# Performance work log

Measured on AMD Instinct MI355X. Metric: run time of the kernel, lower is better.

## Reference

```python
import jax, jax.numpy as jnp
import numpy as np

EPS_RMS = 1e-6
EPS_Q = 1e-5


def _weight_quant(w):
    # BitNet b1.58-style ternary weight quantization with mean-abs scale
    scale = 1.0 / jnp.clip(jnp.mean(jnp.abs(w)), EPS_Q)
    wq = jnp.clip(jnp.round(w * scale), -1.0, 1.0) / scale
    return w + jax.lax.stop_gradient(wq - w)  # STE


def _activation_quant(x):
    # per-token 8-bit absmax quantization
    scale = 127.0 / jnp.clip(jnp.max(jnp.abs(x), axis=-1, keepdims=True), EPS_Q)
    xq = jnp.clip(jnp.round(x * scale), -128.0, 127.0) / scale
    return x + jax.lax.stop_gradient(xq - x)  # STE


def _rmsnorm(x, weight):
    inv = jax.lax.rsqrt(jnp.mean(x * x, axis=-1, keepdims=True) + EPS_RMS)
    return x * inv * weight


def setup_inputs() -> dict:
    key = jax.random.key(0)
    k1, k2, k3 = jax.random.split(key, 3)
    B, S, D, CD = 8, 4096, 1024, 1024
    x = jax.random.normal(k1, (B, S, D), dtype=jnp.float32)
    c = jax.random.normal(k2, (B, CD), dtype=jnp.float32)
    # NOTE: the module zero-inits proj; we use small random weights so the
    # quantized conditioning path is numerically exercised.
    w_proj = jax.random.normal(k3, (2 * D, CD), dtype=jnp.float32) * 0.02
    b_proj = jnp.zeros((2 * D,), dtype=jnp.float32)
    rms_weight = jnp.ones((D,), dtype=jnp.float32)
    return {"x": x, "c": c, "w_proj": w_proj, "b_proj": b_proj, "rms_weight": rms_weight}


def reference(x, c, w_proj, b_proj, rms_weight):
    if c.ndim == 2:
        c = c[:, None, :]  # [B, 1, cond_dim]
    # BitLinear: quantized activations x quantized ternary weights
    cq = _activation_quant(c)
    wq = _weight_quant(w_proj)
    emb = jnp.einsum('btc,dc->btd', cq, wq) + b_proj  # [B, 1, 2*dim]
    scale, shift = jnp.split(emb, 2, axis=-1)
    xn = _rmsnorm(x, rms_weight)
    return xn * (1.0 + scale) + shift
```

## Files before the change

### kernel.cpp

```cpp
#include <hip/hip_runtime.h>
#include <math.h>


constexpr int Bn = 8;
constexpr int Dn = 1024;
constexpr int TWO_D = 2048;
constexpr int OFF_PART = 0;
constexpr int OFF_CQ   = 4096;
constexpr int OFF_G    = 16384;
constexpr int OFF_SH   = 24576;

using f4 = __attribute__((ext_vector_type(4))) float;

__device__ __forceinline__ float wsumf(float v) {
#pragma unroll
    for (int o = 32; o > 0; o >>= 1) v += __shfl_xor(v, o, 64);
    return v;
}
__device__ __forceinline__ float wmaxf(float v) {
#pragma unroll
    for (int o = 32; o > 0; o >>= 1) v = fmaxf(v, __shfl_xor(v, o, 64));
    return v;
}
__device__ __forceinline__ float qclip(float v, float s, float lo, float hi) {
    return fminf(fmaxf(rintf(v * s), lo), hi);
}
__device__ __forceinline__ float maxabs4(f4 v) {
    return fmaxf(fmaxf(fabsf(v.x), fabsf(v.y)), fmaxf(fabsf(v.z), fabsf(v.w)));
}
__device__ __forceinline__ float sumsq4(f4 v) {
    return v.x*v.x + v.y*v.y + v.z*v.z + v.w*v.w;
}

__global__ void k_pre(const float* __restrict__ w, const float* __restrict__ c,
                      float* __restrict__ part, float* __restrict__ cq) {
    int tid = threadIdx.x;
    if (blockIdx.x < TWO_D) {
        f4 v = *(const f4*)(w + (size_t)blockIdx.x * 1024 + (size_t)tid * 4);
        float s = wsumf(fabsf(v.x) + fabsf(v.y) + fabsf(v.z) + fabsf(v.w));
        __shared__ float lds[4];
        if ((tid & 63) == 0) lds[tid >> 6] = s;
        __syncthreads();
        if (tid == 0) part[blockIdx.x] = lds[0] + lds[1] + lds[2] + lds[3];
    } else {
        int b = blockIdx.x - TWO_D;
        f4 v = ((const f4*)(c + (size_t)b * Dn))[tid];
        float m = wmaxf(maxabs4(v));
        __shared__ float lm[4];
        if ((tid & 63) == 0) lm[tid >> 6] = m;
        __syncthreads();
        float mx = fmaxf(fmaxf(lm[0], lm[1]), fmaxf(lm[2], lm[3]));
        float scale = 127.0f / fmaxf(mx, 1e-5f);
        float inv = 1.0f / scale;
        f4 q;
        q.x = qclip(v.x, scale, -128.f, 127.f) * inv;
        q.y = qclip(v.y, scale, -128.f, 127.f) * inv;
        q.z = qclip(v.z, scale, -128.f, 127.f) * inv;
        q.w = qclip(v.w, scale, -128.f, 127.f) * inv;
        ((f4*)(cq + (size_t)b * Dn))[tid] = q;
    }
}

__global__ void k_emb(const float* __restrict__ w, const float* __restrict__ bp,
                      const float* __restrict__ cq, const float* __restrict__ part,
                      const float* __restrict__ rw,
                      float* __restrict__ g, float* __restrict__ sh) {
    int tid = threadIdx.x;
    float s = 0.0f;
#pragma unroll
    for (int k = 0; k < 8; ++k) s += part[tid + k * 256];
    s = wsumf(s);
    __shared__ float lds[4];
    if ((tid & 63) == 0) lds[tid >> 6] = s;
    __syncthreads();
    float mw = fmaxf((lds[0] + lds[1] + lds[2] + lds[3]) * (1.0f / 2097152.0f), 1e-5f);
    float sw = 1.0f / mw;

    int lane = tid & 63;
    int d = (blockIdx.x * blockDim.x + tid) >> 6;
    const float* wr = w + (size_t)d * 1024 + (size_t)lane * 16;
    float t[16];
#pragma unroll
    for (int j = 0; j < 16; j += 4) {
        f4 v = *(const f4*)(wr + j);
        t[j + 0] = qclip(v.x, sw, -1.f, 1.f);
        t[j + 1] = qclip(v.y, sw, -1.f, 1.f);
        t[j + 2] = qclip(v.z, sw, -1.f, 1.f);
        t[j + 3] = qclip(v.w, sw, -1.f, 1.f);
    }
    float acc[Bn];
#pragma unroll
    for (int b = 0; b < Bn; ++b) {
        const float* cr = cq + (size_t)b * Dn + (size_t)lane * 16;
        float dot = 0.0f;
#pragma unroll
        for (int j = 0; j < 16; j += 4) {
            f4 u = *(const f4*)(cr + j);
            dot += t[j + 0] * u.x + t[j + 1] * u.y + t[j + 2] * u.z + t[j + 3] * u.w;
        }
        acc[b] = dot;
    }
#pragma unroll
    for (int o = 32; o > 0; o >>= 1) {
#pragma unroll
        for (int b = 0; b < Bn; ++b) acc[b] += __shfl_xor(acc[b], o, 64);
    }
    if (lane == 0) {
        float bias = bp[d];
        if (d < Dn) {
            float rwd = rw[d];
#pragma unroll
            for (int b = 0; b < Bn; ++b)
                g[b * Dn + d] = rwd * (1.0f + (acc[b] * mw + bias));
        } else {
#pragma unroll
            for (int b = 0; b < Bn; ++b)
                sh[b * Dn + (d - Dn)] = acc[b] * mw + bias;
        }
    }
}

__global__ void __launch_bounds__(256) k_main(
        const float* __restrict__ x, const float* __restrict__ g,
        const float* __restrict__ sh, float* __restrict__ out) {
    int tid  = threadIdx.x;
    int lane = tid & 63;
    int row0 = (blockIdx.x * 4 + (tid >> 6)) * 4;
    int b    = row0 >> 12;

    const f4* gv = (const f4*)(g  + (size_t)b * Dn);
    const f4* hv = (const f4*)(sh + (size_t)b * Dn);
    f4 g0 = gv[lane], g1 = gv[lane+64], g2 = gv[lane+128], g3 = gv[lane+192];
    f4 h0 = hv[lane], h1 = hv[lane+64], h2 = hv[lane+128], h3 = hv[lane+192];

#pragma unroll
    for (int p = 0; p < 2; ++p) {
        int row = row0 + p * 2;
        const f4* xa = (const f4*)(x + (size_t)row * Dn);
        const f4* xb = xa + 256;
        f4 a0 = xa[lane], a1 = xa[lane+64], a2 = xa[lane+128], a3 = xa[lane+192];
        f4 b0 = xb[lane], b1 = xb[lane+64], b2 = xb[lane+128], b3 = xb[lane+192];
        float sa = sumsq4(a0) + sumsq4(a1) + sumsq4(a2) + sumsq4(a3);
        float sb = sumsq4(b0) + sumsq4(b1) + sumsq4(b2) + sumsq4(b3);
#pragma unroll
        for (int o = 32; o > 0; o >>= 1) {
            sa += __shfl_xor(sa, o, 64);
            sb += __shfl_xor(sb, o, 64);
        }
        float ia = rsqrtf(sa * (1.0f / 1024.0f) + 1e-6f);
        float ib = rsqrtf(sb * (1.0f / 1024.0f) + 1e-6f);
        f4* oa = (f4*)(out + (size_t)row * Dn);
        f4* ob = oa + 256;
        f4 o0;
        o0.x = a0.x*ia*g0.x + h0.x; o0.y = a0.y*ia*g0.y + h0.y;
        o0.z = a0.z*ia*g0.z + h0.z; o0.w = a0.w*ia*g0.w + h0.w;
        oa[lane] = o0;
        o0.x = a1.x*ia*g1.x + h1.x; o0.y = a1.y*ia*g1.y + h1.y;
        o0.z = a1.z*ia*g1.z + h1.z; o0.w = a1.w*ia*g1.w + h1.w;
        oa[lane+64] = o0;
        o0.x = a2.x*ia*g2.x + h2.x; o0.y = a2.y*ia*g2.y + h2.y;
        o0.z = a2.z*ia*g2.z + h2.z; o0.w = a2.w*ia*g2.w + h2.w;
        oa[lane+128] = o0;
        o0.x = a3.x*ia*g3.x + h3.x; o0.y = a3.y*ia*g3.y + h3.y;
        o0.z = a3.z*ia*g3.z + h3.z; o0.w = a3.w*ia*g3.w + h3.w;
        oa[lane+192] = o0;
        o0.x = b0.x*ib*g0.x + h0.x; o0.y = b0.y*ib*g0.y + h0.y;
        o0.z = b0.z*ib*g0.z + h0.z; o0.w = b0.w*ib*g0.w + h0.w;
        ob[lane] = o0;
        o0.x = b1.x*ib*g1.x + h1.x; o0.y = b1.y*ib*g1.y + h1.y;
        o0.z = b1.z*ib*g1.z + h1.z; o0.w = b1.w*ib*g1.w + h1.w;
        ob[lane+64] = o0;
        o0.x = b2.x*ib*g2.x + h2.x; o0.y = b2.y*ib*g2.y + h2.y;
        o0.z = b2.z*ib*g2.z + h2.z; o0.w = b2.w*ib*g2.w + h2.w;
        ob[lane+128] = o0;
        o0.x = b3.x*ib*g3.x + h3.x; o0.y = b3.y*ib*g3.y + h3.y;
        o0.z = b3.z*ib*g3.z + h3.z; o0.w = b3.w*ib*g3.w + h3.w;
        ob[lane+192] = o0;
    }
}

extern "C" void kernel_launch(void* const* d_in, const int* in_sizes, int n_in,
                              void* d_out, int out_size, void* d_ws, size_t ws_size,
                              hipStream_t stream) {
    const float* x  = (const float*)d_in[0];
    const float* c  = (const float*)d_in[1];
    const float* w  = (const float*)d_in[2];
    const float* bp = (const float*)d_in[3];
    const float* rw = (const float*)d_in[4];
    float* out = (float*)d_out;
    float* ws  = (float*)d_ws;

    float* part = ws + OFF_PART;
    float* cq   = ws + OFF_CQ;
    float* g    = ws + OFF_G;
    float* sh   = ws + OFF_SH;

    k_pre <<<TWO_D + Bn, 256, 0, stream>>>(w, c, part, cq);
    k_emb <<<TWO_D / 4, 256, 0, stream>>>(w, bp, cq, part, rw, g, sh);
    k_main<<<2048, 256, 0, stream>>>(x, g, sh, out);
}
```

Measured before the change: 61.04 us.

## Fuse three kernels into one cooperative kernel with grid-wide syncs

Merges the weight-abs partial sum, activation quantization, embedding projection and the main RMSNorm/modulation pass into a single cooperative launch of 2048 blocks separated by two grid.sync barriers. The three-kernel path is kept as a fallback when occupancy is too low or the cooperative launch fails. The aim is to remove two kernel launch gaps. In exchange it adds grid-barrier cost, an occupancy query on every call, and a launch-bounds hint that may constrain registers in the main phase.

After: 62.05 us. No clear change (+1.6%).

```diff
diff --git a/kernel.cpp b/kernel.cpp
--- a/kernel.cpp
+++ b/kernel.cpp
@@ -1,17 +1,22 @@
 #include <hip/hip_runtime.h>
+#include <hip/hip_cooperative_groups.h>
 #include <math.h>
 
+namespace cg = cooperative_groups;
+
+using f4 = __attribute__((ext_vector_type(4))) float;
 
 constexpr int Bn = 8;
 constexpr int Dn = 1024;
 constexpr int TWO_D = 2048;
+constexpr int NTHR = 256;
+constexpr int NBLK = 2048;
+
 constexpr int OFF_PART = 0;
 constexpr int OFF_CQ   = 4096;
 constexpr int OFF_G    = 16384;
 constexpr int OFF_SH   = 24576;
 
-using f4 = __attribute__((ext_vector_type(4))) float;
-
 __device__ __forceinline__ float wsumf(float v) {
 #pragma unroll
     for (int o = 32; o > 0; o >>= 1) v += __shfl_xor(v, o, 64);
@@ -32,61 +37,66 @@
     return v.x*v.x + v.y*v.y + v.z*v.z + v.w*v.w;
 }
 
-__global__ void k_pre(const float* __restrict__ w, const float* __restrict__ c,
-                      float* __restrict__ part, float* __restrict__ cq) {
+
+__device__ __forceinline__ void phase_wpart(const float* __restrict__ w,
+                                            float* __restrict__ part, int ch) {
     int tid = threadIdx.x;
-    if (blockIdx.x < TWO_D) {
-        f4 v = *(const f4*)(w + (size_t)blockIdx.x * 1024 + (size_t)tid * 4);
-        float s = wsumf(fabsf(v.x) + fabsf(v.y) + fabsf(v.z) + fabsf(v.w));
-        __shared__ float lds[4];
-        if ((tid & 63) == 0) lds[tid >> 6] = s;
-        __syncthreads();
-        if (tid == 0) part[blockIdx.x] = lds[0] + lds[1] + lds[2] + lds[3];
-    } else {
-        int b = blockIdx.x - TWO_D;
-        f4 v = ((const f4*)(c + (size_t)b * Dn))[tid];
-        float m = wmaxf(maxabs4(v));
-        __shared__ float lm[4];
-        if ((tid & 63) == 0) lm[tid >> 6] = m;
-        __syncthreads();
-        float mx = fmaxf(fmaxf(lm[0], lm[1]), fmaxf(lm[2], lm[3]));
-        float scale = 127.0f / fmaxf(mx, 1e-5f);
-        float inv = 1.0f / scale;
-        f4 q;
-        q.x = qclip(v.x, scale, -128.f, 127.f) * inv;
-        q.y = qclip(v.y, scale, -128.f, 127.f) * inv;
-        q.z = qclip(v.z, scale, -128.f, 127.f) * inv;
-        q.w = qclip(v.w, scale, -128.f, 127.f) * inv;
-        ((f4*)(cq + (size_t)b * Dn))[tid] = q;
-    }
-}
-
-__global__ void k_emb(const float* __restrict__ w, const float* __restrict__ bp,
-                      const float* __restrict__ cq, const float* __restrict__ part,
-                      const float* __restrict__ rw,
-                      float* __restrict__ g, float* __restrict__ sh) {
+    __shared__ float lds[4];
+    f4 v = *(const f4*)(w + (size_t)ch * 1024 + (size_t)tid * 4);
+    float s = wsumf(fabsf(v.x) + fabsf(v.y) + fabsf(v.z) + fabsf(v.w));
+    if ((tid & 63) == 0) lds[tid >> 6] = s;
+    __syncthreads();
+    if (tid == 0) part[ch] = lds[0] + lds[1] + lds[2] + lds[3];
+    __syncthreads();
+}
+
+__device__ __forceinline__ void phase_cq(const float* __restrict__ c,
+                                         float* __restrict__ cq, int b) {
     int tid = threadIdx.x;
+    __shared__ float lm[4];
+    f4 v = ((const f4*)(c + (size_t)b * Dn))[tid];
+    float m = wmaxf(maxabs4(v));
+    if ((tid & 63) == 0) lm[tid >> 6] = m;
+    __syncthreads();
+    float mx = fmaxf(fmaxf(lm[0], lm[1]), fmaxf(lm[2], lm[3]));
+    float scale = 127.0f / fmaxf(mx, 1e-5f);
+    float inv = 1.0f / scale;
+    f4 q;
+    q.x = qclip(v.x, scale, -128.f, 127.f) * inv;
+    q.y = qclip(v.y, scale, -128.f, 127.f) * inv;
+    q.z = qclip(v.z, scale, -128.f, 127.f) * inv;
+    q.w = qclip(v.w, scale, -128.f, 127.f) * inv;
+    ((f4*)(cq + (size_t)b * Dn))[tid] = q;
+}
+
+__device__ __forceinline__ void phase_emb(const float* __restrict__ w,
+                                          const float* __restrict__ bp,
+                                          const float* __restrict__ cq,
+                                          const float* __restrict__ part,
+                                          const float* __restrict__ rw,
+                                          float* __restrict__ g,
+                                          float* __restrict__ sh, int blk) {
+    int tid = threadIdx.x, lane = tid & 63, widx = tid >> 6;
+    __shared__ float lds2[4];
     float s = 0.0f;
 #pragma unroll
     for (int k = 0; k < 8; ++k) s += part[tid + k * 256];
     s = wsumf(s);
-    __shared__ float lds[4];
-    if ((tid & 63) == 0) lds[tid >> 6] = s;
-    __syncthreads();
-    float mw = fmaxf((lds[0] + lds[1] + lds[2] + lds[3]) * (1.0f / 2097152.0f), 1e-5f);
+    if (lane == 0) lds2[widx] = s;
+    __syncthreads();
+    float mw = fmaxf((lds2[0]+lds2[1]+lds2[2]+lds2[3]) * (1.0f / 2097152.0f), 1e-5f);
     float sw = 1.0f / mw;
 
-    int lane = tid & 63;
-    int d = (blockIdx.x * blockDim.x + tid) >> 6;
-    const float* wr = w + (size_t)d * 1024 + (size_t)lane * 16;
+    int d = blk * 4 + widx;
+    const float* wr = w + (size_t)d * Dn + (size_t)lane * 16;
     float t[16];
 #pragma unroll
     for (int j = 0; j < 16; j += 4) {
         f4 v = *(const f4*)(wr + j);
-        t[j + 0] = qclip(v.x, sw, -1.f, 1.f);
-        t[j + 1] = qclip(v.y, sw, -1.f, 1.f);
-        t[j + 2] = qclip(v.z, sw, -1.f, 1.f);
-        t[j + 3] = qclip(v.w, sw, -1.f, 1.f);
+        t[j+0] = qclip(v.x, sw, -1.f, 1.f);
+        t[j+1] = qclip(v.y, sw, -1.f, 1.f);
+        t[j+2] = qclip(v.z, sw, -1.f, 1.f);
+        t[j+3] = qclip(v.w, sw, -1.f, 1.f);
     }
     float acc[Bn];
 #pragma unroll
@@ -96,7 +106,7 @@
 #pragma unroll
         for (int j = 0; j < 16; j += 4) {
             f4 u = *(const f4*)(cr + j);
-            dot += t[j + 0] * u.x + t[j + 1] * u.y + t[j + 2] * u.z + t[j + 3] * u.w;
+            dot += t[j+0]*u.x + t[j+1]*u.y + t[j+2]*u.z + t[j+3]*u.w;
         }
         acc[b] = dot;
     }
@@ -120,14 +130,12 @@
     }
 }
 
-__global__ void __launch_bounds__(256) k_main(
-        const float* __restrict__ x, const float* __restrict__ g,
-        const float* __restrict__ sh, float* __restrict__ out) {
-    int tid  = threadIdx.x;
-    int lane = tid & 63;
-    int row0 = (blockIdx.x * 4 + (tid >> 6)) * 4;
-    int b    = row0 >> 12;
-
+__device__ __forceinline__ void phase_main(const float* __restrict__ x,
+                                           const float* __restrict__ g,
+                                           const float* __restrict__ sh,
+                                           float* __restrict__ out,
+                                           int row0, int lane) {
+    int b = row0 >> 12;
     const f4* gv = (const f4*)(g  + (size_t)b * Dn);
     const f4* hv = (const f4*)(sh + (size_t)b * Dn);
     f4 g0 = gv[lane], g1 = gv[lane+64], g2 = gv[lane+128], g3 = gv[lane+192];
@@ -179,6 +187,49 @@
     }
 }
 
+
+__global__ void __launch_bounds__(NTHR, 8) k_fused(
+    const float* __restrict__ x, const float* __restrict__ c,
+    const float* __restrict__ w, const float* __restrict__ bp,
+    const float* __restrict__ rw, float* __restrict__ part,
+    float* __restrict__ cq, float* __restrict__ g,
+    float* __restrict__ sh, float* __restrict__ out)
+{
+    cg::grid_group grid = cg::this_grid();
+    const int tid = threadIdx.x, lane = tid & 63, widx = tid >> 6;
+    const int blk = blockIdx.x;
+
+    phase_wpart(w, part, blk);
+    if (blk < Bn) phase_cq(c, cq, blk);
+    grid.sync();
+
+    if (blk < 512) phase_emb(w, bp, cq, part, rw, g, sh, blk);
+    grid.sync();
+
+    phase_main(x, g, sh, out, (blk * 4 + widx) * 4, lane);
+}
+
+
+__global__ void k_pre(const float* __restrict__ w, const float* __restrict__ c,
+                      float* __restrict__ part, float* __restrict__ cq) {
+    if (blockIdx.x < TWO_D) phase_wpart(w, part, blockIdx.x);
+    else                    phase_cq(c, cq, blockIdx.x - TWO_D);
+}
+
+__global__ void k_emb(const float* __restrict__ w, const float* __restrict__ bp,
+                      const float* __restrict__ cq, const float* __restrict__ part,
+                      const float* __restrict__ rw,
+                      float* __restrict__ g, float* __restrict__ sh) {
+    phase_emb(w, bp, cq, part, rw, g, sh, blockIdx.x);
+}
+
+__global__ void __launch_bounds__(256) k_main(
+        const float* __restrict__ x, const float* __restrict__ g,
+        const float* __restrict__ sh, float* __restrict__ out) {
+    phase_main(x, g, sh, out, (blockIdx.x * 4 + (threadIdx.x >> 6)) * 4,
+               threadIdx.x & 63);
+}
+
 extern "C" void kernel_launch(void* const* d_in, const int* in_sizes, int n_in,
                               void* d_out, int out_size, void* d_ws, size_t ws_size,
                               hipStream_t stream) {
@@ -187,15 +238,28 @@
     const float* w  = (const float*)d_in[2];
     const float* bp = (const float*)d_in[3];
     const float* rw = (const float*)d_in[4];
-    float* out = (float*)d_out;
-    float* ws  = (float*)d_ws;
+    float* outp = (float*)d_out;
+    float* ws   = (float*)d_ws;
 
     float* part = ws + OFF_PART;
     float* cq   = ws + OFF_CQ;
     float* g    = ws + OFF_G;
     float* sh   = ws + OFF_SH;
 
-    k_pre <<<TWO_D + Bn, 256, 0, stream>>>(w, c, part, cq);
-    k_emb <<<TWO_D / 4, 256, 0, stream>>>(w, bp, cq, part, rw, g, sh);
-    k_main<<<2048, 256, 0, stream>>>(x, g, sh, out);
-}
+    int perCU = 0;
+    hipError_t qerr = hipOccupancyMaxActiveBlocksPerMultiprocessor(
+        &perCU, (const void*)k_fused, NTHR, 0);
+    bool done = false;
+    if (qerr == hipSuccess && perCU * 256 >= NBLK) {
+        void* args[] = { (void*)&x, (void*)&c, (void*)&w, (void*)&bp, (void*)&rw,
+                         (void*)&part, (void*)&cq, (void*)&g, (void*)&sh, (void*)&outp };
+        hipError_t err = hipLaunchCooperativeKernel((const void*)k_fused, dim3(NBLK),
+                                                    dim3(NTHR), args, 0, stream);
+        done = (err == hipSuccess);
+    }
+    if (!done) {
+        k_pre <<<TWO_D + Bn, 256, 0, stream>>>(w, c, part, cq);
+        k_emb <<<512, 256, 0, stream>>>(w, bp, cq, part, rw, g, sh);
+        k_main<<<2048, 256, 0, stream>>>(x, g, sh, outp);
+    }
+}
```

## Move RMS norm statistics into the weight-reduction pre-pass and apply in final kernel

Applied to the files above, without the earlier changes.

The per-row sum of squares of x is now computed in the first kernel, alongside the weight abs-sum partials and the activation quantization, and the per-row inverse norms are written to workspace. The final kernel only loads the stored inverse norm and applies scale and shift. The aim is to take the reduction off the critical path after the embedding kernel, but x is now read twice (once in each pass), which doubles input traffic on a bandwidth-bound op. A fallback path keeps the original schedule when the workspace is too small.

New measurement: 79.07 us. 29.5% more time.

```diff
diff --git a/kernel.cpp b/kernel.cpp
--- a/kernel.cpp
+++ b/kernel.cpp
@@ -9,6 +9,8 @@
 constexpr int OFF_CQ   = 4096;
 constexpr int OFF_G    = 16384;
 constexpr int OFF_SH   = 24576;
+constexpr int OFF_INV  = 32768;
+constexpr size_t WS_NEED = (size_t)(OFF_INV + 32768) * 4;
 
 using f4 = __attribute__((ext_vector_type(4))) float;
 
@@ -32,34 +34,70 @@
     return v.x*v.x + v.y*v.y + v.z*v.z + v.w*v.w;
 }
 
-__global__ void k_pre(const float* __restrict__ w, const float* __restrict__ c,
-                      float* __restrict__ part, float* __restrict__ cq) {
+
+__device__ __forceinline__ void body_wpart(const float* __restrict__ w,
+                                           float* __restrict__ part, int ch) {
     int tid = threadIdx.x;
-    if (blockIdx.x < TWO_D) {
-        f4 v = *(const f4*)(w + (size_t)blockIdx.x * 1024 + (size_t)tid * 4);
-        float s = wsumf(fabsf(v.x) + fabsf(v.y) + fabsf(v.z) + fabsf(v.w));
-        __shared__ float lds[4];
-        if ((tid & 63) == 0) lds[tid >> 6] = s;
-        __syncthreads();
-        if (tid == 0) part[blockIdx.x] = lds[0] + lds[1] + lds[2] + lds[3];
-    } else {
-        int b = blockIdx.x - TWO_D;
-        f4 v = ((const f4*)(c + (size_t)b * Dn))[tid];
-        float m = wmaxf(maxabs4(v));
-        __shared__ float lm[4];
-        if ((tid & 63) == 0) lm[tid >> 6] = m;
-        __syncthreads();
-        float mx = fmaxf(fmaxf(lm[0], lm[1]), fmaxf(lm[2], lm[3]));
-        float scale = 127.0f / fmaxf(mx, 1e-5f);
-        float inv = 1.0f / scale;
-        f4 q;
-        q.x = qclip(v.x, scale, -128.f, 127.f) * inv;
-        q.y = qclip(v.y, scale, -128.f, 127.f) * inv;
-        q.z = qclip(v.z, scale, -128.f, 127.f) * inv;
-        q.w = qclip(v.w, scale, -128.f, 127.f) * inv;
-        ((f4*)(cq + (size_t)b * Dn))[tid] = q;
-    }
-}
+    __shared__ float lds[4];
+    f4 v = *(const f4*)(w + (size_t)ch * 1024 + (size_t)tid * 4);
+    float s = wsumf(fabsf(v.x) + fabsf(v.y) + fabsf(v.z) + fabsf(v.w));
+    if ((tid & 63) == 0) lds[tid >> 6] = s;
+    __syncthreads();
+    if (tid == 0) part[ch] = lds[0] + lds[1] + lds[2] + lds[3];
+    __syncthreads();
+}
+
+__device__ __forceinline__ void body_cq(const float* __restrict__ c,
+                                        float* __restrict__ cq, int b) {
+    int tid = threadIdx.x;
+    __shared__ float lm[4];
+    f4 v = ((const f4*)(c + (size_t)b * Dn))[tid];
+    float m = wmaxf(maxabs4(v));
+    if ((tid & 63) == 0) lm[tid >> 6] = m;
+    __syncthreads();
+    float mx = fmaxf(fmaxf(lm[0], lm[1]), fmaxf(lm[2], lm[3]));
+    float scale = 127.0f / fmaxf(mx, 1e-5f);
+    float inv = 1.0f / scale;
+    f4 q;
+    q.x = qclip(v.x, scale, -128.f, 127.f) * inv;
+    q.y = qclip(v.y, scale, -128.f, 127.f) * inv;
+    q.z = qclip(v.z, scale, -128.f, 127.f) * inv;
+    q.w = qclip(v.w, scale, -128.f, 127.f) * inv;
+    ((f4*)(cq + (size_t)b * Dn))[tid] = q;
+}
+
+
+__global__ void __launch_bounds__(256) k_pass1(
+    const float* __restrict__ x, const float* __restrict__ w,
+    const float* __restrict__ c, float* __restrict__ part,
+    float* __restrict__ cq, float* __restrict__ inv) {
+    int tid = threadIdx.x, lane = tid & 63, widx = tid >> 6, blk = blockIdx.x;
+
+    body_wpart(w, part, blk);
+    if (blk < Bn) body_cq(c, cq, blk);
+
+    int row0 = (blk * 4 + widx) * 4;
+#pragma unroll
+    for (int p = 0; p < 2; ++p) {
+        int row = row0 + p * 2;
+        const f4* xa = (const f4*)(x + (size_t)row * Dn);
+        const f4* xb = xa + 256;
+        f4 a0 = xa[lane], a1 = xa[lane+64], a2 = xa[lane+128], a3 = xa[lane+192];
+        f4 b0 = xb[lane], b1 = xb[lane+64], b2 = xb[lane+128], b3 = xb[lane+192];
+        float sa = sumsq4(a0) + sumsq4(a1) + sumsq4(a2) + sumsq4(a3);
+        float sb = sumsq4(b0) + sumsq4(b1) + sumsq4(b2) + sumsq4(b3);
+#pragma unroll
+        for (int o = 32; o > 0; o >>= 1) {
+            sa += __shfl_xor(sa, o, 64);
+            sb += __shfl_xor(sb, o, 64);
+        }
+        if (lane == 0) {
+            inv[row]     = rsqrtf(sa * (1.0f / 1024.0f) + 1e-6f);
+            inv[row + 1] = rsqrtf(sb * (1.0f / 1024.0f) + 1e-6f);
+        }
+    }
+}
+
 
 __global__ void k_emb(const float* __restrict__ w, const float* __restrict__ bp,
                       const float* __restrict__ cq, const float* __restrict__ part,
@@ -120,19 +158,78 @@
     }
 }
 
-__global__ void __launch_bounds__(256) k_main(
+
+__global__ void __launch_bounds__(256) k_apply(
+        const float* __restrict__ x, const float* __restrict__ inv,
+        const float* __restrict__ g, const float* __restrict__ sh,
+        float* __restrict__ out) {
+    int tid  = threadIdx.x;
+    int lane = tid & 63;
+    int row0 = (blockIdx.x * 4 + (tid >> 6)) * 4;
+    int b    = row0 >> 12;
+
+    const f4* gv = (const f4*)(g  + (size_t)b * Dn);
+    const f4* hv = (const f4*)(sh + (size_t)b * Dn);
+    f4 g0 = gv[lane], g1 = gv[lane+64], g2 = gv[lane+128], g3 = gv[lane+192];
+    f4 h0 = hv[lane], h1 = hv[lane+64], h2 = hv[lane+128], h3 = hv[lane+192];
+
+#pragma unroll
+    for (int p = 0; p < 2; ++p) {
+        int row = row0 + p * 2;
+        float ia = inv[row];
+        float ib = inv[row + 1];
+        const f4* xa = (const f4*)(x + (size_t)row * Dn);
+        const f4* xb = xa + 256;
+        f4 a0 = xa[lane], a1 = xa[lane+64], a2 = xa[lane+128], a3 = xa[lane+192];
+        f4 b0 = xb[lane], b1 = xb[lane+64], b2 = xb[lane+128], b3 = xb[lane+192];
+        f4* oa = (f4*)(out + (size_t)row * Dn);
+        f4* ob = oa + 256;
+        f4 o0;
+        o0.x = a0.x*ia*g0.x + h0.x; o0.y = a0.y*ia*g0.y + h0.y;
+        o0.z = a0.z*ia*g0.z + h0.z; o0.w = a0.w*ia*g0.w + h0.w;
+        oa[lane] = o0;
+        o0.x = a1.x*ia*g1.x + h1.x; o0.y = a1.y*ia*g1.y + h1.y;
+        o0.z = a1.z*ia*g1.z + h1.z; o0.w = a1.w*ia*g1.w + h1.w;
+        oa[lane+64] = o0;
+        o0.x = a2.x*ia*g2.x + h2.x; o0.y = a2.y*ia*g2.y + h2.y;
+        o0.z = a2.z*ia*g2.z + h2.z; o0.w = a2.w*ia*g2.w + h2.w;
+        oa[lane+128] = o0;
+        o0.x = a3.x*ia*g3.x + h3.x; o0.y = a3.y*ia*g3.y + h3.y;
+        o0.z = a3.z*ia*g3.z + h3.z; o0.w = a3.w*ia*g3.w + h3.w;
+        oa[lane+192] = o0;
+        o0.x = b0.x*ib*g0.x + h0.x; o0.y = b0.y*ib*g0.y + h0.y;
+        o0.z = b0.z*ib*g0.z + h0.z; o0.w = b0.w*ib*g0.w + h0.w;
+        ob[lane] = o0;
+        o0.x = b1.x*ib*g1.x + h1.x; o0.y = b1.y*ib*g1.y + h1.y;
+        o0.z = b1.z*ib*g1.z + h1.z; o0.w = b1.w*ib*g1.w + h1.w;
+        ob[lane+64] = o0;
+        o0.x = b2.x*ib*g2.x + h2.x; o0.y = b2.y*ib*g2.y + h2.y;
+        o0.z = b2.z*ib*g2.z + h2.z; o0.w = b2.w*ib*g2.w + h2.w;
+        ob[lane+128] = o0;
+        o0.x = b3.x*ib*g3.x + h3.x; o0.y = b3.y*ib*g3.y + h3.y;
+        o0.z = b3.z*ib*g3.z + h3.z; o0.w = b3.w*ib*g3.w + h3.w;
+        ob[lane+192] = o0;
+    }
+}
+
+
+__global__ void k_pre_fb(const float* __restrict__ w, const float* __restrict__ c,
+                         float* __restrict__ part, float* __restrict__ cq) {
+    if (blockIdx.x < TWO_D) body_wpart(w, part, blockIdx.x);
+    else                    body_cq(c, cq, blockIdx.x - TWO_D);
+}
+
+__global__ void __launch_bounds__(256) k_main_fb(
         const float* __restrict__ x, const float* __restrict__ g,
         const float* __restrict__ sh, float* __restrict__ out) {
     int tid  = threadIdx.x;
     int lane = tid & 63;
     int row0 = (blockIdx.x * 4 + (tid >> 6)) * 4;
     int b    = row0 >> 12;
-
     const f4* gv = (const f4*)(g  + (size_t)b * Dn);
     const f4* hv = (const f4*)(sh + (size_t)b * Dn);
     f4 g0 = gv[lane], g1 = gv[lane+64], g2 = gv[lane+128], g3 = gv[lane+192];
     f4 h0 = hv[lane], h1 = hv[lane+64], h2 = hv[lane+128], h3 = hv[lane+192];
-
 #pragma unroll
     for (int p = 0; p < 2; ++p) {
         int row = row0 + p * 2;
@@ -194,8 +291,15 @@
     float* cq   = ws + OFF_CQ;
     float* g    = ws + OFF_G;
     float* sh   = ws + OFF_SH;
-
-    k_pre <<<TWO_D + Bn, 256, 0, stream>>>(w, c, part, cq);
-    k_emb <<<TWO_D / 4, 256, 0, stream>>>(w, bp, cq, part, rw, g, sh);
-    k_main<<<2048, 256, 0, stream>>>(x, g, sh, out);
-}
+    float* inv  = ws + OFF_INV;
+
+    if (ws_size >= WS_NEED) {
+        k_pass1<<<TWO_D, 256, 0, stream>>>(x, w, c, part, cq, inv);
+        k_emb  <<<512, 256, 0, stream>>>(w, bp, cq, part, rw, g, sh);
+        k_apply<<<2048, 256, 0, stream>>>(x, inv, g, sh, out);
+    } else {
+        k_pre_fb<<<TWO_D + Bn, 256, 0, stream>>>(w, c, part, cq);
+        k_emb   <<<512, 256, 0, stream>>>(w, bp, cq, part, rw, g, sh);
+        k_main_fb<<<2048, 256, 0, stream>>>(x, g, sh, out);
+    }
+}
```
